# Optimization experiments

Hardware: AMD Instinct MI355X
Metric: run time of the kernel (lower is better)

Reference implementation:

```python
import jax, jax.numpy as jnp
import numpy as np

FACTOR = 2  # upsample factor per spatial dim


def setup_inputs() -> dict:
    key = jax.random.key(0)
    k1, k2, k3 = jax.random.split(key, 3)
    B, C_in, C_out, H, W_ = 8, 128, 128, 64, 64
    x = jax.random.normal(k1, (B, C_in, H, W_), dtype=jnp.float32)
    # conv3x3 params (OIHW), fan-in scaled init like torch Conv2d default scale
    fan_in = C_in * 3 * 3
    W = jax.random.normal(k2, (C_out, C_in, 3, 3), dtype=jnp.float32) / np.sqrt(fan_in)
    b = jax.random.normal(k3, (C_out,), dtype=jnp.float32) * 0.01
    return {"x": x, "W": W, "b": b}


def reference(x, W, b):
    h = jnp.repeat(jnp.repeat(x, FACTOR, axis=2), FACTOR, axis=3)  # [B,C,2H,2W]
    # conv3x3: stride 1, padding 1
    out = jax.lax.conv_general_dilated(
        h, W,
        window_strides=(1, 1),
        padding=((1, 1), (1, 1)),
        dimension_numbers=("NCHW", "OIHW", "NCHW"),
    )
    return out + b[None, :, None, None]
```

## Files before the change

kernel.cpp:

```cpp
#include <hip/hip_runtime.h>
#include <stdint.h>

typedef short bf16x8 __attribute__((ext_vector_type(8)));
typedef float f32x4 __attribute__((ext_vector_type(4)));

#define NCI 128
#define NCO 128
#define HIN 64
#define HP  66
#define NB  8

__device__ __forceinline__ unsigned short f32_to_bf16(float f) {
    union { float f; uint32_t u; } v; v.f = f;
    return (unsigned short)((v.u + 0x7FFFu + ((v.u >> 16) & 1u)) >> 16);
}

__device__ __forceinline__ void gl_lds16(const void* g, void* l) {
    __builtin_amdgcn_global_load_lds(
        (const __attribute__((address_space(1))) unsigned int*)g,
        (__attribute__((address_space(3))) unsigned int*)l, 16, 0, 0);
}

__device__ __forceinline__ void vmw0() {
    asm volatile("s_waitcnt vmcnt(0)" ::: "memory");
}
__device__ __forceinline__ void lkw0() {
    asm volatile("s_waitcnt lgkmcnt(0)" ::: "memory");
}
__device__ __forceinline__ void barx() {
    asm volatile("" ::: "memory");
    __builtin_amdgcn_s_barrier();
    asm volatile("" ::: "memory");
}

__device__ __forceinline__ float weff_sum(const float* wp, int py, int px, int ty, int tx) {
    float s = 0.f;
    #pragma unroll
    for (int ky = 0; ky < 3; ++ky) {
        bool iy = (py == 0) ? (ty == 0 ? (ky == 0) : (ky >= 1))
                            : (ty == 0 ? (ky <= 1) : (ky == 2));
        if (!iy) continue;
        #pragma unroll
        for (int kx = 0; kx < 3; ++kx) {
            bool ix = (px == 0) ? (tx == 0 ? (kx == 0) : (kx >= 1))
                                : (tx == 0 ? (kx <= 1) : (kx == 2));
            if (ix) s += wp[ky * 3 + kx];
        }
    }
    return s;
}

__global__ __launch_bounds__(256) void prep_kernel(
        const float* __restrict__ W, const float* __restrict__ x,
        unsigned short* __restrict__ Aw4, unsigned short* __restrict__ xq) {
    if (blockIdx.x < 1024) {
        int idx = blockIdx.x * 256 + threadIdx.x;
        int e   = idx & 7;
        int rl  = (idx >> 3) & 15;
        int pl  = (idx >> 7) & 3;
        int f   = (idx >> 9) & 1;
        int wmq = (idx >> 10) & 3;
        int kt  = (idx >> 12) & 15;
        int par = idx >> 16;
        int co = wmq * 32 + f * 16 + rl;
        int k  = kt * 32 + pl * 8 + e;
        int tap = k >> 7, ci = k & 127;
        Aw4[idx] = f32_to_bf16(weff_sum(W + (co * NCI + ci) * 9,
                                        par >> 1, par & 1, tap >> 1, tap & 1));
    } else {
        const int bb = blockIdx.x - 1024;
        const int b = bb / HP, hp = bb % HP;
        const int t = threadIdx.x;
        if (hp == 0 || hp == HP - 1) {
            bf16x8 z = (bf16x8){0, 0, 0, 0, 0, 0, 0, 0};
            for (int i = t; i < 4 * HP * 4; i += 256) {
                int g = i / (HP * 4), rem = i % (HP * 4);
                unsigned short* dst = xq +
                    ((((size_t)(b * 4 + g) * HP + hp) * HP) << 5) + rem * 8;
                *(bf16x8*)dst = z;
            }
            return;
        }
        const int h = hp - 1;
        if (t < 32) {
            bf16x8 z = (bf16x8){0, 0, 0, 0, 0, 0, 0, 0};
            int g = t >> 3, wpc = ((t >> 2) & 1) * (HP - 1), q = t & 3;
            unsigned short* dst = xq +
                ((((size_t)(b * 4 + g) * HP + hp) * HP + wpc) << 5) + q * 8;
            *(bf16x8*)dst = z;
        }
        const int w = t & 63, g = t >> 6;
        const float* src = x + ((size_t)(b * NCI + g * 32) * (HIN * HIN)) + h * HIN + w;
        unsigned short* dst = xq +
            ((((size_t)(b * 4 + g) * HP + hp) * HP + (w + 1)) << 5);
        #pragma unroll
        for (int q = 0; q < 4; ++q) {
            bf16x8 v;
            #pragma unroll
            for (int j = 0; j < 8; ++j)
                v[j] = (short)f32_to_bf16(src[(size_t)(q * 8 + j) * (HIN * HIN)]);
            *(bf16x8*)(dst + q * 8) = v;
        }
    }
}

__global__ __launch_bounds__(512, 4) void upconv9_kernel(
        const unsigned short* __restrict__ xq, const unsigned short* __restrict__ Aw4,
        const float* __restrict__ bv, float* __restrict__ out) {
    __shared__ __align__(16) unsigned short smem[25344];
    const int d = blockIdx.x;
    const int dsw = (d & 7) * 64 + (d >> 3);
    const int tile = dsw >> 1, py = dsw & 1;
    const int bi = tile >> 5;
    const int oy0 = (tile & 31) * 2;
    const int tid = threadIdx.x, lane = tid & 63, wv = tid >> 6;
    const int pxw = wv & 1, wmq = wv >> 1;
    const int rl = lane & 15, pl = lane >> 4;
    const int par = py * 2 + pxw;

    #pragma unroll
    for (int i = 0; i < 7; ++i) {
        int dd = i * 512 + tid;
        if (dd < 3168) {
            int cell = dd >> 4, chq = dd & 15;
            int ry = cell / 66, colg = cell - ry * 66;
            int chunk = chq ^ (colg & 15);
            const unsigned short* gb = xq +
                ((((size_t)(bi * 4 + (chunk >> 2)) * HP + (oy0 + py + ry)) * HP + colg) << 5)
                + (chunk & 3) * 8;
            gl_lds16(gb, &smem[dd * 8]);
        }
    }

    f32x4 acc[2][8];
    #pragma unroll
    for (int i = 0; i < 2; ++i)
        #pragma unroll
        for (int j = 0; j < 8; ++j)
            acc[i][j] = (f32x4){0.f, 0.f, 0.f, 0.f};

    bf16x8 A0[2], A1[2];
    auto loadA = [&](bf16x8* Ad, int kt) {
        const unsigned short* p = Aw4 + ((((par * 16 + kt) * 4 + wmq)) << 10) + lane * 8;
        Ad[0] = *(const bf16x8*)p;
        Ad[1] = *(const bf16x8*)(p + 512);
    };

    loadA(A0, 0);
    vmw0();
    barx();

    #pragma unroll 2
    for (int kt = 0; kt < 16; ++kt) {
        if (kt < 15) loadA((kt & 1) ? A0 : A1, kt + 1);
        const bf16x8* Ac = (kt & 1) ? A1 : A0;
        const int ty = kt >> 3, tx = (kt >> 2) & 1, cq = kt & 3;
        #pragma unroll
        for (int half = 0; half < 2; ++half) {
            bf16x8 bfr[4];
            #pragma unroll
            for (int f = 0; f < 4; ++f) {
                int n = (half * 4 + f) * 16 + rl;
                int ry = (n >> 6) + ty;
                int colg = (n & 63) + pxw + tx;
                int chq = (cq * 4 + pl) ^ (colg & 15);
                bfr[f] = *(const bf16x8*)&smem[(((ry * 66 + colg) << 4) + chq) * 8];
            }
            #pragma unroll
            for (int fm = 0; fm < 2; ++fm)
                #pragma unroll
                for (int f = 0; f < 4; ++f)
                    acc[fm][half * 4 + f] = __builtin_amdgcn_mfma_f32_16x16x32_bf16(
                        Ac[fm], bfr[f], acc[fm][half * 4 + f], 0, 0, 0);
        }
    }

    barx();

    float* lf = (float*)smem;
    const int co_l = tid >> 4;
    const int rr = (tid >> 3) & 1, x16 = (tid & 7) * 16;
    const int yy = 2 * (oy0 + rr) + py;

    #pragma unroll
    for (int b = 0; b < 4; ++b) {
        if (wmq == b) {
            #pragma unroll
            for (int fm = 0; fm < 2; ++fm)
                #pragma unroll
                for (int fn = 0; fn < 8; ++fn) {
                    int n = fn * 16 + rl;
                    int r = n >> 6, xx = 2 * (n & 63) + pxw;
                    #pragma unroll
                    for (int j = 0; j < 4; ++j)
                        lf[(fm * 16 + pl * 4 + j) * 264 + r * 132 + xx] = acc[fm][fn][j];
                }
        }
        lkw0();
        barx();
        const int co = b * 32 + co_l;
        const float bb = bv[co];
        float* op = out + (((size_t)bi * NCO + co) * 128 + yy) * 128 + x16;
        const float* sp = lf + co_l * 264 + rr * 132 + x16;
        #pragma unroll
        for (int q = 0; q < 4; ++q) {
            f32x4 v = *(const f32x4*)(sp + q * 4);
            v[0] += bb; v[1] += bb; v[2] += bb; v[3] += bb;
            *(f32x4*)(op + q * 4) = v;
        }
        if (b < 3) barx();
    }
}

__global__ void weff_flat_kernel(const float* __restrict__ W,
                                 unsigned short* __restrict__ Aw) {
    int idx = blockIdx.x * 256 + threadIdx.x;
    int par = idx >> 16;
    int co  = (idx >> 9) & 127;
    int k   = idx & 511;
    int tap = k >> 7, ci = k & 127;
    Aw[idx] = f32_to_bf16(weff_sum(W + (co * NCI + ci) * 9,
                                   par >> 1, par & 1, tap >> 1, tap & 1));
}

__global__ __launch_bounds__(256) void upconv_fb_kernel(
        const float* __restrict__ x, const unsigned short* __restrict__ Aw,
        const float* __restrict__ bv, float* __restrict__ out) {
    __shared__ __align__(16) unsigned short A_lds[128 * 32];
    __shared__ __align__(16) unsigned short B_lds[128 * 32];
    const int par = blockIdx.y, py = par >> 1, px = par & 1;
    const int s0 = blockIdx.x * 128;
    const int bimg = s0 >> 12;
    const int oy0 = (s0 >> 6) & 63;
    const int tid = threadIdx.x;
    const int lane = tid & 63, wave = tid >> 6;
    const int wm = wave >> 1, wn = wave & 1;
    const float* xb = x + bimg * (NCI * HIN * HIN);
    f32x4 acc[4][4];
    #pragma unroll
    for (int i = 0; i < 4; ++i)
        #pragma unroll
        for (int j = 0; j < 4; ++j)
            acc[i][j] = (f32x4){0.f, 0.f, 0.f, 0.f};
    for (int kt = 0; kt < 16; ++kt) {
        const int tap = kt >> 2, ci0 = (kt & 3) * 32;
        const int ty = tap >> 1, tx = tap & 1;
        #pragma unroll
        for (int i = 0; i < 2; ++i) {
            int c = i * 256 + tid;
            *(bf16x8*)(&A_lds[c * 8]) = *(const bf16x8*)(Aw +
                ((par * 128 + (c >> 2)) * 512 + kt * 32 + (c & 3) * 8));
        }
        #pragma unroll
        for (int i = 0; i < 2; ++i) {
            int tsk = i * 256 + tid;
            int n = tsk & 127, kg = tsk >> 7;
            int r = n >> 6, ox = n & 63;
            int row = oy0 + r - 1 + py + ty;
            int col = ox - 1 + px + tx;
            bool ok = (row >= 0) & (row < HIN) & (col >= 0) & (col < HIN);
            const float* xp = xb + (((ci0 + kg * 8) * HIN + row) * HIN + col);
            bf16x8 v;
            #pragma unroll
            for (int q = 0; q < 8; ++q) {
                float f = ok ? xp[q * (HIN * HIN)] : 0.f;
                v[q] = (short)f32_to_bf16(f);
            }
            *(bf16x8*)(&B_lds[n * 32 + kg * 8]) = v;
        }
        __syncthreads();
        const int seg = (lane >> 4) * 8, rl2 = lane & 15;
        bf16x8 af[4], bfr[4];
        #pragma unroll
        for (int f = 0; f < 4; ++f)
            af[f] = *(const bf16x8*)(&A_lds[(wm * 64 + f * 16 + rl2) * 32 + seg]);
        #pragma unroll
        for (int f = 0; f < 4; ++f)
            bfr[f] = *(const bf16x8*)(&B_lds[(wn * 64 + f * 16 + rl2) * 32 + seg]);
        #pragma unroll
        for (int fm = 0; fm < 4; ++fm)
            #pragma unroll
            for (int fn = 0; fn < 4; ++fn)
                acc[fm][fn] = __builtin_amdgcn_mfma_f32_16x16x32_bf16(
                    af[fm], bfr[fn], acc[fm][fn], 0, 0, 0);
        __syncthreads();
    }
    #pragma unroll
    for (int fm = 0; fm < 4; ++fm) {
        const int co_b = wm * 64 + fm * 16 + (lane >> 4) * 4;
        float bias4[4];
        #pragma unroll
        for (int j = 0; j < 4; ++j) bias4[j] = bv[co_b + j];
        #pragma unroll
        for (int fn = 0; fn < 4; ++fn) {
            int n = wn * 64 + fn * 16 + (lane & 15);
            int s = s0 + n;
            int ox = s & 63, oy = (s >> 6) & 63, bi2 = s >> 12;
            int yy = 2 * oy + py, xx = 2 * ox + px;
            float* op = out + ((size_t)bi2 * 128 * 128 * 128) + (size_t)yy * 128 + xx;
            #pragma unroll
            for (int j = 0; j < 4; ++j)
                op[(size_t)(co_b + j) * (128 * 128)] = acc[fm][fn][j] + bias4[j];
        }
    }
}

extern "C" void kernel_launch(void* const* d_in, const int* in_sizes, int n_in,
                              void* d_out, int out_size, void* d_ws, size_t ws_size,
                              hipStream_t stream) {
    const float* x  = (const float*)d_in[0];
    const float* W  = (const float*)d_in[1];
    const float* bv = (const float*)d_in[2];
    float* out = (float*)d_out;
    unsigned short* Aw = (unsigned short*)d_ws;
    const size_t aw_bytes = (size_t)4 * 16 * 4 * 2 * 512 * sizeof(unsigned short);
    const size_t xq_bytes = (size_t)NB * 4 * HP * HP * 32 * sizeof(unsigned short);

    if (ws_size >= aw_bytes + xq_bytes) {
        unsigned short* xq = (unsigned short*)((char*)d_ws + aw_bytes);
        prep_kernel<<<1024 + NB * HP, 256, 0, stream>>>(W, x, Aw, xq);
        upconv9_kernel<<<512, 512, 0, stream>>>(xq, Aw, bv, out);
    } else {
        weff_flat_kernel<<<1024, 256, 0, stream>>>(W, Aw);
        upconv_fb_kernel<<<dim3(256, 4), 256, 0, stream>>>(x, Aw, bv, out);
    }
}
```

Baseline: 47.46 us.

## Retile waves to 64x64 output blocks with 2x2 M/N wave split

Changes the per-wave MFMA tile from 32 output channels x 128 pixels to 64 channels x 64 pixels. The 8 waves are now split over parity, a channel half and a pixel row. Each wave reads 4 B fragments from LDS per k-step instead of 8 and loads 4 A fragments from global memory instead of 2, which cuts LDS read traffic per MFMA. The weight prep layout and the epilogue staging are re-indexed to match, and s_setprio is raised around the MFMA loop. The trade-off is more global A loads and more A registers per wave, which may raise register pressure under the 4-block launch bound.

```diff
diff --git a/kernel.cpp b/kernel.cpp
--- a/kernel.cpp
+++ b/kernel.cpp
@@ -52,20 +52,20 @@
 
 __global__ __launch_bounds__(256) void prep_kernel(
         const float* __restrict__ W, const float* __restrict__ x,
-        unsigned short* __restrict__ Aw4, unsigned short* __restrict__ xq) {
+        unsigned short* __restrict__ Aw5, unsigned short* __restrict__ xq) {
     if (blockIdx.x < 1024) {
         int idx = blockIdx.x * 256 + threadIdx.x;
         int e   = idx & 7;
         int rl  = (idx >> 3) & 15;
         int pl  = (idx >> 7) & 3;
-        int f   = (idx >> 9) & 1;
-        int wmq = (idx >> 10) & 3;
+        int f   = (idx >> 9) & 3;
+        int wm  = (idx >> 11) & 1;
         int kt  = (idx >> 12) & 15;
         int par = idx >> 16;
-        int co = wmq * 32 + f * 16 + rl;
+        int co = wm * 64 + f * 16 + rl;
         int k  = kt * 32 + pl * 8 + e;
         int tap = k >> 7, ci = k & 127;
-        Aw4[idx] = f32_to_bf16(weff_sum(W + (co * NCI + ci) * 9,
+        Aw5[idx] = f32_to_bf16(weff_sum(W + (co * NCI + ci) * 9,
                                         par >> 1, par & 1, tap >> 1, tap & 1));
     } else {
         const int bb = blockIdx.x - 1024;
@@ -104,8 +104,8 @@
     }
 }
 
-__global__ __launch_bounds__(512, 4) void upconv9_kernel(
-        const unsigned short* __restrict__ xq, const unsigned short* __restrict__ Aw4,
+__global__ __launch_bounds__(512, 4) void upconv10_kernel(
+        const unsigned short* __restrict__ xq, const unsigned short* __restrict__ Aw5,
         const float* __restrict__ bv, float* __restrict__ out) {
     __shared__ __align__(16) unsigned short smem[25344];
     const int d = blockIdx.x;
@@ -114,7 +114,7 @@
     const int bi = tile >> 5;
     const int oy0 = (tile & 31) * 2;
     const int tid = threadIdx.x, lane = tid & 63, wv = tid >> 6;
-    const int pxw = wv & 1, wmq = wv >> 1;
+    const int pxw = wv & 1, wm = (wv >> 1) & 1, wn = wv >> 2;
     const int rl = lane & 15, pl = lane >> 4;
     const int par = py * 2 + pxw;
 
@@ -132,18 +132,19 @@
         }
     }
 
-    f32x4 acc[2][8];
-    #pragma unroll
-    for (int i = 0; i < 2; ++i)
-        #pragma unroll
-        for (int j = 0; j < 8; ++j)
+    f32x4 acc[4][4];
+    #pragma unroll
+    for (int i = 0; i < 4; ++i)
+        #pragma unroll
+        for (int j = 0; j < 4; ++j)
             acc[i][j] = (f32x4){0.f, 0.f, 0.f, 0.f};
 
-    bf16x8 A0[2], A1[2];
-    auto loadA = [&](bf16x8* Ad, int kt) {
-        const unsigned short* p = Aw4 + ((((par * 16 + kt) * 4 + wmq)) << 10) + lane * 8;
-        Ad[0] = *(const bf16x8*)p;
-        Ad[1] = *(const bf16x8*)(p + 512);
+    bf16x8 A0[4], A1[4];
+    auto loadA = [&](bf16x8* Ad, int kt2) {
+        const unsigned short* p = Aw5 + (((par * 16 + kt2) * 2 + wm) << 11) + lane * 8;
+        #pragma unroll
+        for (int f = 0; f < 4; ++f)
+            Ad[f] = *(const bf16x8*)(p + f * 512);
     };
 
     loadA(A0, 0);
@@ -155,50 +156,44 @@
         if (kt < 15) loadA((kt & 1) ? A0 : A1, kt + 1);
         const bf16x8* Ac = (kt & 1) ? A1 : A0;
         const int ty = kt >> 3, tx = (kt >> 2) & 1, cq = kt & 3;
-        #pragma unroll
-        for (int half = 0; half < 2; ++half) {
-            bf16x8 bfr[4];
-            #pragma unroll
-            for (int f = 0; f < 4; ++f) {
-                int n = (half * 4 + f) * 16 + rl;
-                int ry = (n >> 6) + ty;
-                int colg = (n & 63) + pxw + tx;
-                int chq = (cq * 4 + pl) ^ (colg & 15);
-                bfr[f] = *(const bf16x8*)&smem[(((ry * 66 + colg) << 4) + chq) * 8];
-            }
-            #pragma unroll
-            for (int fm = 0; fm < 2; ++fm)
-                #pragma unroll
-                for (int f = 0; f < 4; ++f)
-                    acc[fm][half * 4 + f] = __builtin_amdgcn_mfma_f32_16x16x32_bf16(
-                        Ac[fm], bfr[f], acc[fm][half * 4 + f], 0, 0, 0);
-        }
+        const int ry = wn + ty;
+        __builtin_amdgcn_s_setprio(1);
+        #pragma unroll
+        for (int f = 0; f < 4; ++f) {
+            const int colg = f * 16 + rl + pxw + tx;
+            const int chq = (cq * 4 + pl) ^ (colg & 15);
+            bf16x8 bfr = *(const bf16x8*)&smem[(((ry * 66 + colg) << 4) + chq) * 8];
+            #pragma unroll
+            for (int fm = 0; fm < 4; ++fm)
+                acc[fm][f] = __builtin_amdgcn_mfma_f32_16x16x32_bf16(
+                    Ac[fm], bfr, acc[fm][f], 0, 0, 0);
+        }
+        __builtin_amdgcn_s_setprio(0);
     }
 
     barx();
 
     float* lf = (float*)smem;
     const int co_l = tid >> 4;
-    const int rr = (tid >> 3) & 1, x16 = (tid & 7) * 16;
+    const int rem = tid & 15, rr = rem >> 3, x16 = (rem & 7) * 16;
+    const int co_g = (co_l >> 4) * 64 + (co_l & 15);
     const int yy = 2 * (oy0 + rr) + py;
 
     #pragma unroll
-    for (int b = 0; b < 4; ++b) {
-        if (wmq == b) {
-            #pragma unroll
-            for (int fm = 0; fm < 2; ++fm)
-                #pragma unroll
-                for (int fn = 0; fn < 8; ++fn) {
-                    int n = fn * 16 + rl;
-                    int r = n >> 6, xx = 2 * (n & 63) + pxw;
-                    #pragma unroll
-                    for (int j = 0; j < 4; ++j)
-                        lf[(fm * 16 + pl * 4 + j) * 264 + r * 132 + xx] = acc[fm][fn][j];
-                }
+    for (int fm = 0; fm < 4; ++fm) {
+        #pragma unroll
+        for (int fn = 0; fn < 4; ++fn) {
+            int n = wn * 64 + fn * 16 + rl;
+            int r = n >> 6, xx = 2 * (n & 63) + pxw;
+            #pragma unroll
+            for (int j = 0; j < 4; ++j) {
+                int col = wm * 16 + pl * 4 + j;
+                lf[col * 264 + r * 132 + xx] = acc[fm][fn][j];
+            }
         }
         lkw0();
         barx();
-        const int co = b * 32 + co_l;
+        const int co = co_g + fm * 16;
         const float bb = bv[co];
         float* op = out + (((size_t)bi * NCO + co) * 128 + yy) * 128 + x16;
         const float* sp = lf + co_l * 264 + rr * 132 + x16;
@@ -208,7 +203,7 @@
             v[0] += bb; v[1] += bb; v[2] += bb; v[3] += bb;
             *(f32x4*)(op + q * 4) = v;
         }
-        if (b < 3) barx();
+        if (fm < 3) barx();
     }
 }
 
@@ -313,13 +308,13 @@
     const float* bv = (const float*)d_in[2];
     float* out = (float*)d_out;
     unsigned short* Aw = (unsigned short*)d_ws;
-    const size_t aw_bytes = (size_t)4 * 16 * 4 * 2 * 512 * sizeof(unsigned short);
+    const size_t aw_bytes = (size_t)4 * 16 * 2 * 2048 * sizeof(unsigned short);
     const size_t xq_bytes = (size_t)NB * 4 * HP * HP * 32 * sizeof(unsigned short);
 
     if (ws_size >= aw_bytes + xq_bytes) {
         unsigned short* xq = (unsigned short*)((char*)d_ws + aw_bytes);
         prep_kernel<<<1024 + NB * HP, 256, 0, stream>>>(W, x, Aw, xq);
-        upconv9_kernel<<<512, 512, 0, stream>>>(xq, Aw, bv, out);
+        upconv10_kernel<<<512, 512, 0, stream>>>(xq, Aw, bv, out);
     } else {
         weff_flat_kernel<<<1024, 256, 0, stream>>>(W, Aw);
         upconv_fb_kernel<<<dim3(256, 4), 256, 0, stream>>>(x, Aw, bv, out);
```

Result: no change. 48.11 us (+1.4%).
